# Optimization experiments

Hardware: AMD Instinct MI355X
Metric: run time of the kernel (lower is better)

Reference implementation:

```python
import jax, jax.numpy as jnp
import numpy as np

D_MODEL = 1024
NHEAD = 16
HEAD_DIM = D_MODEL // NHEAD


def setup_inputs() -> dict:
    key = jax.random.key(0)
    ks = jax.random.split(key, 11)
    B, S = 4, 2048
    s = 1.0 / np.sqrt(D_MODEL)
    return {
        "q": jax.random.normal(ks[0], (B, S, D_MODEL), jnp.float32),
        "k": jax.random.normal(ks[1], (B, S, D_MODEL), jnp.float32),
        "v": jax.random.normal(ks[2], (B, S, D_MODEL), jnp.float32),
        "Wq": jax.random.normal(ks[3], (D_MODEL, D_MODEL), jnp.float32) * s,
        "bq": jnp.zeros((D_MODEL,), jnp.float32),
        "Wk": jax.random.normal(ks[4], (D_MODEL, D_MODEL), jnp.float32) * s,
        "bk": jnp.zeros((D_MODEL,), jnp.float32),
        "Wv": jax.random.normal(ks[5], (D_MODEL, D_MODEL), jnp.float32) * s,
        "bv": jnp.zeros((D_MODEL,), jnp.float32),
        "Wo": jax.random.normal(ks[6], (D_MODEL, D_MODEL), jnp.float32) * s,
        "bo": jnp.zeros((D_MODEL,), jnp.float32),
    }


def reference(q, k, v, Wq, bq, Wk, bk, Wv, bv, Wo, bo):
    B, S, _ = q.shape
    H, Dh = NHEAD, HEAD_DIM

    def proj(x, W, b):  # nn.Linear: x @ W.T + b, then split heads -> [B,H,S,Dh]
        y = x @ W.T + b
        return y.reshape(B, S, H, Dh).transpose(0, 2, 1, 3)

    qh = proj(q, Wq, bq)
    kh = proj(k, Wk, bk)
    vh = proj(v, Wv, bv)

    scores = jnp.einsum("bhsd,bhtd->bhst", qh, kh) / jnp.sqrt(jnp.float32(Dh))
    attn = jax.nn.softmax(scores, axis=-1)
    out = jnp.einsum("bhst,bhtd->bhsd", attn, vh)  # [B,H,S,Dh]
    out = out.transpose(0, 2, 1, 3).reshape(B, S, H * Dh)
    return out @ Wo.T + bo
```

## Files before the change

kernel.cpp:

```cpp
#include <hip/hip_runtime.h>


typedef short bf16x8 __attribute__((ext_vector_type(8)));
typedef short bf16x4 __attribute__((ext_vector_type(4)));
typedef float f32x4 __attribute__((ext_vector_type(4)));
typedef float f32x16 __attribute__((ext_vector_type(16)));
typedef unsigned int u32x4 __attribute__((ext_vector_type(4)));

__device__ __forceinline__ short f2bf(float x) {
    union { float f; unsigned int u; } un; un.f = x;
    unsigned int u = un.u;
    return (short)(unsigned short)((u + 0x7fffu + ((u >> 16) & 1u)) >> 16);
}

__device__ __forceinline__ void gll16(const void* g, void* l) {
    __builtin_amdgcn_global_load_lds(
        (const __attribute__((address_space(1))) void*)g,
        (__attribute__((address_space(3))) void*)l, 16, 0, 0);
}

__device__ __forceinline__ void plswap(unsigned& a, unsigned& b) {
    asm("v_permlane32_swap_b32 %0, %1" : "+v"(a), "+v"(b));
}

struct CvtArgs { const float* s[4]; unsigned short* d[4]; int n4; };
__global__ __launch_bounds__(256) void cvt_bf16(CvtArgs ca) {
    const float* s = ca.s[blockIdx.y];
    unsigned short* d = ca.d[blockIdx.y];
    int i = blockIdx.x * blockDim.x + threadIdx.x;
    int stride = gridDim.x * blockDim.x;
    const float4* s4 = reinterpret_cast<const float4*>(s);
    bf16x4* d4 = reinterpret_cast<bf16x4*>(d);
    for (; i < ca.n4; i += stride) {
        float4 x = s4[i];
        bf16x4 y;
        y[0] = f2bf(x.x); y[1] = f2bf(x.y); y[2] = f2bf(x.z); y[3] = f2bf(x.w);
        d4[i] = y;
    }
}

__device__ __forceinline__ void gemm_core(const unsigned short* __restrict__ A,
                                          const unsigned short* __restrict__ W,
                                          const float* __restrict__ bias,
                                          float scale, void* __restrict__ out,
                                          int mode) {
    __shared__ unsigned short As[128 * 64];
    __shared__ unsigned short Bs[128 * 64];
    const int tid = threadIdx.x;
    const int m0 = (mode == 2 ? blockIdx.x : blockIdx.y) * 128;
    const int n0 = (mode == 2 ? blockIdx.y : blockIdx.x) * 128;
    const int wave = tid >> 6, lane = tid & 63;
    const int wm = (wave >> 1) * 64, wn = (wave & 1) * 64;
    const int l15 = lane & 15, quad = lane >> 4;
    const int srow = tid >> 3;
    const int scol = ((tid & 7) ^ (srow & 7)) * 8;
    const int cb = (l15 & 7);

    f32x4 acc[4][4] = {};

    for (int k0 = 0; k0 < 1024; k0 += 64) {
        __syncthreads();
#pragma unroll
        for (int ro = 0; ro < 4; ++ro) {
            gll16(&A[(size_t)(m0 + ro * 32 + srow) * 1024 + k0 + scol], &As[ro * 2048 + tid * 8]);
            gll16(&W[(size_t)(n0 + ro * 32 + srow) * 1024 + k0 + scol], &Bs[ro * 2048 + tid * 8]);
        }
        __syncthreads();
#pragma unroll
        for (int kk = 0; kk < 2; ++kk) {
            const int co = ((4 * kk + quad) ^ cb) * 8;
            bf16x8 a[4], b[4];
#pragma unroll
            for (int i = 0; i < 4; ++i)
                a[i] = *reinterpret_cast<bf16x8*>(&As[(wm + i * 16 + l15) * 64 + co]);
#pragma unroll
            for (int j = 0; j < 4; ++j)
                b[j] = *reinterpret_cast<bf16x8*>(&Bs[(wn + j * 16 + l15) * 64 + co]);
#pragma unroll
            for (int i = 0; i < 4; ++i)
#pragma unroll
                for (int j = 0; j < 4; ++j)
                    acc[i][j] = __builtin_amdgcn_mfma_f32_16x16x32_bf16(a[i], b[j], acc[i][j], 0, 0, 0);
        }
    }

#pragma unroll
    for (int i = 0; i < 4; ++i) {
#pragma unroll
        for (int j = 0; j < 4; ++j) {
#pragma unroll
            for (int r = 0; r < 4; ++r) {
                int m = m0 + wm + i * 16 + quad * 4 + r;
                int n = n0 + wn + j * 16 + l15;
                float val = (acc[i][j][r] + bias[mode == 2 ? m : n]) * scale;
                if (mode == 0) {
                    reinterpret_cast<float*>(out)[(size_t)m * 1024 + n] = val;
                } else if (mode == 1) {
                    int b_ = m >> 11, s = m & 2047, h = n >> 6, d = n & 63;
                    size_t off = (size_t)((b_ * 16 + h) * 2048 + s) * 64 + d;
                    reinterpret_cast<unsigned short*>(out)[off] = (unsigned short)f2bf(val);
                } else {
                    int h = m >> 6, d = m & 63, b_ = n >> 11, s = n & 2047;
                    size_t off = (size_t)((b_ * 16 + h) * 64 + d) * 2048 + s;
                    reinterpret_cast<unsigned short*>(out)[off] = (unsigned short)f2bf(val);
                }
            }
        }
    }
}

struct QkvArgs {
    const unsigned short* A[3];
    const unsigned short* W[3];
    const float* bias[3];
    float scale[3];
    unsigned short* out[3];
    int mode[3];
};
__global__ __launch_bounds__(256) void gemm_qkv(QkvArgs ga) {
    int z = blockIdx.z;
    gemm_core(ga.A[z], ga.W[z], ga.bias[z], ga.scale[z], ga.out[z], ga.mode[z]);
}

__global__ __launch_bounds__(256) void gemm_wo(const unsigned short* __restrict__ A,
                                               const unsigned short* __restrict__ W,
                                               const float* __restrict__ bias,
                                               float* __restrict__ out) {
    gemm_core(A, W, bias, 1.0f, out, 0);
}


#define SOFTMAX_PV(MT, VBASE)                                                        \
    {                                                                                \
        float e[16];                                                                 \
        _Pragma("unroll")                                                            \
        for (int r = 0; r < 16; ++r) e[r] = __builtin_amdgcn_exp2f(sacc[MT][r]);     \
        lacc += ((e[0] + e[1]) + (e[2] + e[3])) + ((e[4] + e[5]) + (e[6] + e[7])) +  \
                ((e[8] + e[9]) + (e[10] + e[11])) + ((e[12] + e[13]) + (e[14] + e[15])); \
        unsigned w[8];                                                               \
        _Pragma("unroll")                                                            \
        for (int t = 0; t < 8; ++t) {                                                \
            union { float f; unsigned u; } a0{e[2 * t]}, a1{e[2 * t + 1]};           \
            w[t] = __builtin_amdgcn_perm(a1.u + 0x8000u, a0.u + 0x8000u, 0x07060302u); \
        }                                                                            \
        plswap(w[0], w[2]); plswap(w[1], w[3]);                                      \
        plswap(w[4], w[6]); plswap(w[5], w[7]);                                      \
        u32x4 t0; t0[0] = w[0]; t0[1] = w[1]; t0[2] = w[2]; t0[3] = w[3];            \
        u32x4 t1; t1[0] = w[4]; t1[1] = w[5]; t1[2] = w[6]; t1[3] = w[7];            \
        bf16x8 pa0 = __builtin_bit_cast(bf16x8, t0);                                 \
        bf16x8 pa1 = __builtin_bit_cast(bf16x8, t1);                                 \
        __builtin_amdgcn_s_setprio(1);                                               \
        _Pragma("unroll")                                                            \
        for (int nt = 0; nt < 2; ++nt) {                                             \
            bf16x8 bv0 = *reinterpret_cast<const bf16x8*>(&(VBASE)[rowoff[nt] + chx[2 * (MT)]]); \
            bf16x8 bv1 = *reinterpret_cast<const bf16x8*>(&(VBASE)[rowoff[nt] + chx[2 * (MT) + 1]]); \
            o[nt] = __builtin_amdgcn_mfma_f32_32x32x16_bf16(pa0, bv0, o[nt], 0, 0, 0); \
            o[nt] = __builtin_amdgcn_mfma_f32_32x32x16_bf16(pa1, bv1, o[nt], 0, 0, 0); \
        }                                                                            \
        __builtin_amdgcn_s_setprio(0);                                               \
    }

#define QK_TILE(KBASE)                                                               \
    {                                                                                \
        f32x16 zz = {};                                                              \
        sacc[0] = zz; sacc[1] = zz;                                                  \
        __builtin_amdgcn_s_setprio(1);                                               \
        _Pragma("unroll")                                                            \
        for (int c = 0; c < 4; ++c) {                                                \
            bf16x8 ak0 = *reinterpret_cast<const bf16x8*>(&(KBASE)[rowoff[0] + chx[c]]); \
            bf16x8 ak1 = *reinterpret_cast<const bf16x8*>(&(KBASE)[rowoff[1] + chx[c]]); \
            sacc[0] = __builtin_amdgcn_mfma_f32_32x32x16_bf16(ak0, qreg[c], sacc[0], 0, 0, 0); \
            sacc[1] = __builtin_amdgcn_mfma_f32_32x32x16_bf16(ak1, qreg[c], sacc[1], 0, 0, 0); \
        }                                                                            \
        __builtin_amdgcn_s_setprio(0);                                               \
    }

__global__ __launch_bounds__(256, 4) void flash_attn(const unsigned short* __restrict__ Qh,
                                                     const unsigned short* __restrict__ Kh,
                                                     const unsigned short* __restrict__ Vt,
                                                     unsigned short* __restrict__ Oa) {
    __shared__ unsigned short Ks[2][64 * 64];
    __shared__ unsigned short Vs[2][64 * 64];
    const int tid = threadIdx.x;
    const int bh = blockIdx.y;
    const int q0 = blockIdx.x * 128;
    const unsigned short* Qb = Qh + (size_t)bh * 2048 * 64;
    const unsigned short* Kb = Kh + (size_t)bh * 2048 * 64;
    const unsigned short* Vb = Vt + (size_t)bh * 64 * 2048;
    const int wave = tid >> 6, lane = tid & 63;
    const int l31 = lane & 31, hi = lane >> 5;
    const int wq = wave * 32;
    const int srow = tid >> 3;
    const int scol = ((tid & 7) ^ (srow & 7)) * 8;

    int chx[4], rowoff[2];
#pragma unroll
    for (int c = 0; c < 4; ++c) chx[c] = ((c * 2 + hi) ^ (l31 & 7)) * 8;
    rowoff[0] = l31 * 64;
    rowoff[1] = (32 + l31) * 64;

    bf16x8 qreg[4];
#pragma unroll
    for (int c = 0; c < 4; ++c)
        qreg[c] = *reinterpret_cast<const bf16x8*>(
            &Qb[(size_t)(q0 + wq + l31) * 64 + c * 16 + hi * 8]);

    f32x16 o[2] = {};
    f32x16 sacc[2];
    float lacc = 0.f;

#pragma unroll
    for (int ro = 0; ro < 2; ++ro) {
        gll16(&Kb[(size_t)(ro * 32 + srow) * 64 + scol], &Ks[0][ro * 2048 + tid * 8]);
        gll16(&Vb[(size_t)(ro * 32 + srow) * 2048 + scol], &Vs[0][ro * 2048 + tid * 8]);
        gll16(&Kb[(size_t)(64 + ro * 32 + srow) * 64 + scol], &Ks[1][ro * 2048 + tid * 8]);
    }
    __syncthreads();
    QK_TILE(Ks[0]);
    __syncthreads();

    for (int it = 0; it < 31; ++it) {
        const int cur = it & 1, nxt = cur ^ 1;
        if (it < 30) {
            const int kvn = (it + 2) * 64;
#pragma unroll
            for (int ro = 0; ro < 2; ++ro)
                gll16(&Kb[(size_t)(kvn + ro * 32 + srow) * 64 + scol], &Ks[cur][ro * 2048 + tid * 8]);
        }
        {
            const int kvn = (it + 1) * 64;
#pragma unroll
            for (int ro = 0; ro < 2; ++ro)
                gll16(&Vb[(size_t)(ro * 32 + srow) * 2048 + kvn + scol], &Vs[nxt][ro * 2048 + tid * 8]);
        }

        SOFTMAX_PV(0, Vs[cur]);
        SOFTMAX_PV(1, Vs[cur]);

        QK_TILE(Ks[nxt]);

        __syncthreads();
    }
    SOFTMAX_PV(0, Vs[1]);
    SOFTMAX_PV(1, Vs[1]);

    float lfull = lacc + __shfl_xor(lacc, 32, 64);
    float rinv = 1.0f / lfull;
    const int b_ = bh >> 4, h = bh & 15;
#pragma unroll
    for (int r = 0; r < 16; ++r) {
        const int qrow = (r & 3) + 8 * (r >> 2) + 4 * hi;
        const float rl = __shfl(rinv, qrow, 64);
        const int s = q0 + wq + qrow;
#pragma unroll
        for (int nt = 0; nt < 2; ++nt) {
            const int d = nt * 32 + l31;
            Oa[(size_t)(b_ * 2048 + s) * 1024 + h * 64 + d] =
                (unsigned short)f2bf(o[nt][r] * rl);
        }
    }
}

extern "C" void kernel_launch(void* const* d_in, const int* in_sizes, int n_in,
                              void* d_out, int out_size, void* d_ws, size_t ws_size,
                              hipStream_t stream) {
    const float* q  = (const float*)d_in[0];
    const float* k  = (const float*)d_in[1];
    const float* v  = (const float*)d_in[2];
    const float* Wq = (const float*)d_in[3];
    const float* bq = (const float*)d_in[4];
    const float* Wk = (const float*)d_in[5];
    const float* bk = (const float*)d_in[6];
    const float* Wv = (const float*)d_in[7];
    const float* bv = (const float*)d_in[8];
    const float* Wo = (const float*)d_in[9];
    const float* bo = (const float*)d_in[10];

    const size_t E = (size_t)8192 * 1024;
    const size_t WE = (size_t)1024 * 1024;
    unsigned short* r0 = (unsigned short*)d_ws;
    unsigned short* r1 = r0 + E;
    unsigned short* r2 = r1 + E;
    unsigned short* r3 = r2 + E;
    unsigned short* wqb = r3 + E;
    unsigned short* wkb = wqb + WE;
    unsigned short* wvb = wkb + WE;
    unsigned short* wob = wvb + WE;

    CvtArgs ca;
    ca.s[0] = q; ca.d[0] = r0;
    ca.s[1] = k; ca.d[1] = r1;
    ca.s[2] = v; ca.d[2] = r2;
    ca.s[3] = q; ca.d[3] = r0;
    ca.n4 = (int)(E / 4);
    cvt_bf16<<<dim3(1024, 3), 256, 0, stream>>>(ca);

    CvtArgs cw;
    cw.s[0] = Wq; cw.d[0] = wqb;
    cw.s[1] = Wk; cw.d[1] = wkb;
    cw.s[2] = Wv; cw.d[2] = wvb;
    cw.s[3] = Wo; cw.d[3] = wob;
    cw.n4 = (int)(WE / 4);
    cvt_bf16<<<dim3(256, 4), 256, 0, stream>>>(cw);

    const float QSCALE = 0.125f * 1.44269504088896340736f;

    QkvArgs ga;
    ga.A[0] = r0;  ga.W[0] = wqb; ga.bias[0] = bq; ga.scale[0] = QSCALE; ga.out[0] = r3; ga.mode[0] = 1;
    ga.A[1] = r1;  ga.W[1] = wkb; ga.bias[1] = bk; ga.scale[1] = 1.0f;   ga.out[1] = r0; ga.mode[1] = 1;
    ga.A[2] = wvb; ga.W[2] = r2;  ga.bias[2] = bv; ga.scale[2] = 1.0f;   ga.out[2] = r1; ga.mode[2] = 2;
    gemm_qkv<<<dim3(8, 64, 3), 256, 0, stream>>>(ga);

    flash_attn<<<dim3(16, 64), 256, 0, stream>>>(r3, r0, r1, r2);
    gemm_wo<<<dim3(8, 64), 256, 0, stream>>>(r2, wob, bo, (float*)d_out);
}
```

Before: 384.2 us.

## Double-buffer LDS tiles in projection GEMM and unify V projection orientation

The GEMM core now keeps two LDS buffers and issues global-to-LDS loads for the next K tile while MFMAs run on the current one, replacing the two-barrier load-then-compute loop. The V projection is no longer computed as a transposed product (Wv as A, activations as B). It is computed in the same orientation as Q and K and scattered into the transposed layout at store time. Doubling LDS to 64KB per block may cut occupancy. The transposed V stores now write scattered 2-byte elements instead of contiguous ones.

```diff
diff --git a/kernel.cpp b/kernel.cpp
--- a/kernel.cpp
+++ b/kernel.cpp
@@ -44,11 +44,10 @@
                                           const float* __restrict__ bias,
                                           float scale, void* __restrict__ out,
                                           int mode) {
-    __shared__ unsigned short As[128 * 64];
-    __shared__ unsigned short Bs[128 * 64];
+    __shared__ unsigned short As[2][128 * 64];
+    __shared__ unsigned short Bs[2][128 * 64];
     const int tid = threadIdx.x;
-    const int m0 = (mode == 2 ? blockIdx.x : blockIdx.y) * 128;
-    const int n0 = (mode == 2 ? blockIdx.y : blockIdx.x) * 128;
+    const int m0 = blockIdx.y * 128, n0 = blockIdx.x * 128;
     const int wave = tid >> 6, lane = tid & 63;
     const int wm = (wave >> 1) * 64, wn = (wave & 1) * 64;
     const int l15 = lane & 15, quad = lane >> 4;
@@ -58,30 +57,40 @@
 
     f32x4 acc[4][4] = {};
 
-    for (int k0 = 0; k0 < 1024; k0 += 64) {
-        __syncthreads();
-#pragma unroll
-        for (int ro = 0; ro < 4; ++ro) {
-            gll16(&A[(size_t)(m0 + ro * 32 + srow) * 1024 + k0 + scol], &As[ro * 2048 + tid * 8]);
-            gll16(&W[(size_t)(n0 + ro * 32 + srow) * 1024 + k0 + scol], &Bs[ro * 2048 + tid * 8]);
-        }
-        __syncthreads();
+#pragma unroll
+    for (int ro = 0; ro < 4; ++ro) {
+        gll16(&A[(size_t)(m0 + ro * 32 + srow) * 1024 + scol], &As[0][ro * 2048 + tid * 8]);
+        gll16(&W[(size_t)(n0 + ro * 32 + srow) * 1024 + scol], &Bs[0][ro * 2048 + tid * 8]);
+    }
+    __syncthreads();
+
+    for (int kt = 0; kt < 16; ++kt) {
+        const int cur = kt & 1;
+        if (kt < 15) {
+            const int k0 = (kt + 1) * 64;
+#pragma unroll
+            for (int ro = 0; ro < 4; ++ro) {
+                gll16(&A[(size_t)(m0 + ro * 32 + srow) * 1024 + k0 + scol], &As[cur ^ 1][ro * 2048 + tid * 8]);
+                gll16(&W[(size_t)(n0 + ro * 32 + srow) * 1024 + k0 + scol], &Bs[cur ^ 1][ro * 2048 + tid * 8]);
+            }
+        }
 #pragma unroll
         for (int kk = 0; kk < 2; ++kk) {
             const int co = ((4 * kk + quad) ^ cb) * 8;
             bf16x8 a[4], b[4];
 #pragma unroll
             for (int i = 0; i < 4; ++i)
-                a[i] = *reinterpret_cast<bf16x8*>(&As[(wm + i * 16 + l15) * 64 + co]);
+                a[i] = *reinterpret_cast<bf16x8*>(&As[cur][(wm + i * 16 + l15) * 64 + co]);
 #pragma unroll
             for (int j = 0; j < 4; ++j)
-                b[j] = *reinterpret_cast<bf16x8*>(&Bs[(wn + j * 16 + l15) * 64 + co]);
+                b[j] = *reinterpret_cast<bf16x8*>(&Bs[cur][(wn + j * 16 + l15) * 64 + co]);
 #pragma unroll
             for (int i = 0; i < 4; ++i)
 #pragma unroll
                 for (int j = 0; j < 4; ++j)
                     acc[i][j] = __builtin_amdgcn_mfma_f32_16x16x32_bf16(a[i], b[j], acc[i][j], 0, 0, 0);
         }
+        __syncthreads();
     }
 
 #pragma unroll
@@ -92,16 +101,14 @@
             for (int r = 0; r < 4; ++r) {
                 int m = m0 + wm + i * 16 + quad * 4 + r;
                 int n = n0 + wn + j * 16 + l15;
-                float val = (acc[i][j][r] + bias[mode == 2 ? m : n]) * scale;
+                float val = (acc[i][j][r] + bias[n]) * scale;
                 if (mode == 0) {
                     reinterpret_cast<float*>(out)[(size_t)m * 1024 + n] = val;
-                } else if (mode == 1) {
+                } else {
                     int b_ = m >> 11, s = m & 2047, h = n >> 6, d = n & 63;
-                    size_t off = (size_t)((b_ * 16 + h) * 2048 + s) * 64 + d;
-                    reinterpret_cast<unsigned short*>(out)[off] = (unsigned short)f2bf(val);
-                } else {
-                    int h = m >> 6, d = m & 63, b_ = n >> 11, s = n & 2047;
-                    size_t off = (size_t)((b_ * 16 + h) * 64 + d) * 2048 + s;
+                    size_t off = (mode == 1)
+                                     ? ((size_t)((b_ * 16 + h) * 2048 + s) * 64 + d)
+                                     : ((size_t)((b_ * 16 + h) * 64 + d) * 2048 + s);
                     reinterpret_cast<unsigned short*>(out)[off] = (unsigned short)f2bf(val);
                 }
             }
@@ -306,9 +313,9 @@
     const float QSCALE = 0.125f * 1.44269504088896340736f;
 
     QkvArgs ga;
-    ga.A[0] = r0;  ga.W[0] = wqb; ga.bias[0] = bq; ga.scale[0] = QSCALE; ga.out[0] = r3; ga.mode[0] = 1;
-    ga.A[1] = r1;  ga.W[1] = wkb; ga.bias[1] = bk; ga.scale[1] = 1.0f;   ga.out[1] = r0; ga.mode[1] = 1;
-    ga.A[2] = wvb; ga.W[2] = r2;  ga.bias[2] = bv; ga.scale[2] = 1.0f;   ga.out[2] = r1; ga.mode[2] = 2;
+    ga.A[0] = r0; ga.W[0] = wqb; ga.bias[0] = bq; ga.scale[0] = QSCALE; ga.out[0] = r3; ga.mode[0] = 1;
+    ga.A[1] = r1; ga.W[1] = wkb; ga.bias[1] = bk; ga.scale[1] = 1.0f;   ga.out[1] = r0; ga.mode[1] = 1;
+    ga.A[2] = r2; ga.W[2] = wvb; ga.bias[2] = bv; ga.scale[2] = 1.0f;   ga.out[2] = r1; ga.mode[2] = 2;
     gemm_qkv<<<dim3(8, 64, 3), 256, 0, stream>>>(ga);
 
     flash_attn<<<dim3(16, 64), 256, 0, stream>>>(r3, r0, r1, r2);
```

Result: faster. 368.6 us (-4.1%).
